# Kernel optimization log

Hardware: AMD Instinct MI355X
Metric: run time of the kernel (lower is better)

## Reference

```python
import jax, jax.numpy as jnp
import numpy as np

N = 100000   # nodes
E = 1600000  # edges per snapshot
S = 4        # snapshots
D = 128      # node_dim
H = 256      # hidden dim
P = 10000    # post nodes


def setup_inputs() -> dict:
    key = jax.random.key(0)
    ks = jax.random.split(key, 11)
    return {
        "node_features": jax.random.normal(ks[0], (N, D), jnp.float32),
        "edge_index": jax.random.randint(ks[1], (S, 2, E), 0, N, dtype=jnp.int32),
        "post_idx": jax.random.randint(ks[2], (P,), 0, N, dtype=jnp.int32),
        "W1": jax.random.normal(ks[3], (D, H), jnp.float32) * (1.0 / np.sqrt(D)),
        "b1": jnp.zeros((H,), jnp.float32),
        "W2": jax.random.normal(ks[4], (H, H), jnp.float32) * (1.0 / np.sqrt(H)),
        "b2": jnp.zeros((H,), jnp.float32),
        "Wc1": jax.random.normal(ks[5], (H, H // 2), jnp.float32) * (1.0 / np.sqrt(H)),
        "bc1": jnp.zeros((H // 2,), jnp.float32),
        "Wc2": jax.random.normal(ks[6], (H // 2, 1), jnp.float32) * (1.0 / np.sqrt(H // 2)),
        "bc2": jnp.zeros((1,), jnp.float32),
    }


def _gcn_conv(x, W, b, src, dst):
    # PyG GCNConv: linear transform, then symmetric-normalized aggregation
    # with self-loops: out_i = sum_j (xW)_j / sqrt(d_i d_j) + (xW)_i / d_i + b
    xw = x @ W                                   # [N, H]
    deg = jnp.ones((N,), xw.dtype).at[dst].add(1.0)  # in-degree + self-loop
    dinv = jax.lax.rsqrt(deg)                    # [N]
    norm = dinv[src] * dinv[dst]                 # [E]
    msg = xw[src] * norm[:, None]                # [E, H] gather + scale
    agg = jax.ops.segment_sum(msg, dst, num_segments=N)  # scatter-add
    agg = agg + xw * (dinv * dinv)[:, None]      # self-loop term
    return agg + b


def reference(node_features, edge_index, post_idx, W1, b1, W2, b2, Wc1, bc1, Wc2, bc2):
    embs = []
    for s in range(S):  # small fixed snapshot loop
        src, dst = edge_index[s, 0], edge_index[s, 1]
        # layer 0: 128->256, relu (dropout identity in eval), no residual (dim change)
        h = jax.nn.relu(_gcn_conv(node_features, W1, b1, src, dst))
        # layer 1 (last): no relu, residual since dims match
        h = _gcn_conv(h, W2, b2, src, dst) + h
        embs.append(h)
    agg = jnp.mean(jnp.stack(embs), axis=0)      # 'mean' snapshot aggregation
    post = agg[post_idx]                         # [P, H]
    hid = jax.nn.relu(post @ Wc1 + bc1)
    logits = (hid @ Wc2 + bc2)[:, 0]
    return jax.nn.sigmoid(logits)
```

## Files before the change

### kernel.cpp

```cpp
#include <hip/hip_runtime.h>
#include <math.h>

#define N_NODES 100000
#define E_EDGES 1600000
#define S_SNAP  4
#define D_IN    128
#define H_DIM   256
#define P_POST  10000
#define SCAN_NBLK ((N_NODES + 255) / 256)
#define NBIN 8
#define BIN_W (N_NODES / NBIN)
#define FILL_CHUNK 2048
#define FILL_NCHUNK ((E_EDGES + FILL_CHUNK - 1) / FILL_CHUNK)

typedef __attribute__((ext_vector_type(8))) short bf16x8;
typedef __attribute__((ext_vector_type(4))) float f32x4;

__device__ __forceinline__ float bf2f(unsigned short u) {
    union { unsigned int i; float f; } v; v.i = ((unsigned int)u) << 16; return v.f;
}
__device__ __forceinline__ unsigned short f2bf(float f) {
    union { float f; unsigned int i; } v; v.f = f;
    unsigned int lsb = (v.i >> 16) & 1u;
    v.i += 0x7fffu + lsb;
    return (unsigned short)(v.i >> 16);
}

__global__ void zero32_kernel(unsigned int* __restrict__ p, int n) {
    int i = blockIdx.x * blockDim.x + threadIdx.x;
    if (i < n) p[i] = 0u;
}

__global__ void hist_kernel(const int* __restrict__ dst, int* __restrict__ deg,
        int* __restrict__ slot) {
    int i = blockIdx.x * blockDim.x + threadIdx.x;
    if (i < E_EDGES) slot[i] = atomicAdd(&deg[dst[i]], 1);
}

__global__ void dinv_kernel(const int* __restrict__ deg, float* __restrict__ dinv) {
    int i = blockIdx.x * blockDim.x + threadIdx.x;
    if (i < N_NODES) dinv[i] = rsqrtf((float)(deg[i] + 1));
}

__global__ __launch_bounds__(256) void scan_part_kernel(const int* __restrict__ deg,
        int* __restrict__ bsum) {
    __shared__ int red[4];
    int i = blockIdx.x * 256 + threadIdx.x;
    int s = (i < N_NODES) ? deg[i] : 0;
    #pragma unroll
    for (int off = 32; off > 0; off >>= 1) s += __shfl_down(s, off, 64);
    int wave = threadIdx.x >> 6, lane = threadIdx.x & 63;
    if (lane == 0) red[wave] = s;
    __syncthreads();
    if (threadIdx.x == 0) bsum[blockIdx.x] = red[0] + red[1] + red[2] + red[3];
}

__global__ __launch_bounds__(512) void scan_top_kernel(const int* __restrict__ bsum,
        int* __restrict__ boff) {
    __shared__ int s[512];
    int t = threadIdx.x;
    s[t] = (t < SCAN_NBLK) ? bsum[t] : 0;
    __syncthreads();
    for (int off = 1; off < 512; off <<= 1) {
        int v = (t >= off) ? s[t - off] : 0;
        __syncthreads();
        s[t] += v;
        __syncthreads();
    }
    if (t < SCAN_NBLK) boff[t] = (t == 0) ? 0 : s[t - 1];
}

__global__ __launch_bounds__(256) void scan_fin_kernel(const int* __restrict__ deg,
        const int* __restrict__ boff, int* __restrict__ rowptr) {
    __shared__ int s[256];
    int b = blockIdx.x, t = threadIdx.x;
    int i = b * 256 + t;
    int v = (i < N_NODES) ? deg[i] : 0;
    s[t] = v;
    __syncthreads();
    for (int off = 1; off < 256; off <<= 1) {
        int u = (t >= off) ? s[t - off] : 0;
        __syncthreads();
        s[t] += u;
        __syncthreads();
    }
    if (i < N_NODES) rowptr[i] = boff[b] + s[t] - v;
    if (i == 0) rowptr[N_NODES] = E_EDGES;
}

__global__ __launch_bounds__(256) void fill_kernel(const int* __restrict__ src,
        const int* __restrict__ dst, const int* __restrict__ slot,
        const int* __restrict__ rowptr, int* __restrict__ csrsrc) {
    int chunk = blockIdx.x >> 3;
    int bin = blockIdx.x & (NBIN - 1);
    int lo = bin * BIN_W, hi = lo + BIN_W;
    int base = chunk * FILL_CHUNK + threadIdx.x;
    #pragma unroll
    for (int k = 0; k < FILL_CHUNK / 256; ++k) {
        int i = base + k * 256;
        if (i < E_EDGES) {
            int d = dst[i];
            if (d >= lo && d < hi) csrsrc[rowptr[d] + slot[i]] = src[i];
        }
    }
}

__global__ __launch_bounds__(256) void gemm_xw1_mfma(const float* __restrict__ A,
        const float* __restrict__ B, unsigned short* __restrict__ C, int M) {
    __shared__ unsigned short As[64][136];
    __shared__ unsigned short Bs[64][136];
    int tid = threadIdx.x;
    int m0 = blockIdx.x * 64, n0 = blockIdx.y * 64;
    {
        int row = tid >> 2, c0 = (tid & 3) * 32;
        int gm = m0 + row;
        #pragma unroll
        for (int i = 0; i < 8; ++i) {
            float4 v = make_float4(0.f, 0.f, 0.f, 0.f);
            if (gm < M) v = *(const float4*)(A + (size_t)gm * D_IN + c0 + i * 4);
            As[row][c0 + i * 4 + 0] = f2bf(v.x);
            As[row][c0 + i * 4 + 1] = f2bf(v.y);
            As[row][c0 + i * 4 + 2] = f2bf(v.z);
            As[row][c0 + i * 4 + 3] = f2bf(v.w);
        }
    }
    {
        int k = tid >> 1, nb = (tid & 1) * 32;
        #pragma unroll
        for (int i = 0; i < 8; ++i) {
            float4 v = *(const float4*)(B + (size_t)k * H_DIM + n0 + nb + i * 4);
            Bs[nb + i * 4 + 0][k] = f2bf(v.x);
            Bs[nb + i * 4 + 1][k] = f2bf(v.y);
            Bs[nb + i * 4 + 2][k] = f2bf(v.z);
            Bs[nb + i * 4 + 3][k] = f2bf(v.w);
        }
    }
    __syncthreads();
    int w = tid >> 6, l = tid & 63;
    int q = l >> 4, mrow = l & 15;
    f32x4 acc[4] = {{0.f,0.f,0.f,0.f},{0.f,0.f,0.f,0.f},{0.f,0.f,0.f,0.f},{0.f,0.f,0.f,0.f}};
    #pragma unroll
    for (int kk = 0; kk < 4; ++kk) {
        bf16x8 a = *(const bf16x8*)&As[16 * w + mrow][kk * 32 + q * 8];
        #pragma unroll
        for (int ct = 0; ct < 4; ++ct) {
            bf16x8 b = *(const bf16x8*)&Bs[ct * 16 + mrow][kk * 32 + q * 8];
            acc[ct] = __builtin_amdgcn_mfma_f32_16x16x32_bf16(a, b, acc[ct], 0, 0, 0);
        }
    }
    #pragma unroll
    for (int ct = 0; ct < 4; ++ct) {
        int col = n0 + ct * 16 + mrow;
        #pragma unroll
        for (int i = 0; i < 4; ++i) {
            int m = m0 + 16 * w + q * 4 + i;
            if (m < M) C[(size_t)m * H_DIM + col] = f2bf(acc[ct][i]);
        }
    }
}

__global__ __launch_bounds__(256) void spmm_l0_kernel(const unsigned short* __restrict__ xw1,
        const float* __restrict__ dinv, const int* __restrict__ rowptr,
        const int* __restrict__ csrsrc, const float* __restrict__ b1,
        unsigned short* __restrict__ h) {
    int r = (blockIdx.x << 2) + (threadIdx.x >> 6);
    int lane = threadIdx.x & 63;
    int e0 = rowptr[r], e1 = rowptr[r + 1];
    float di = dinv[r];
    float4 acc = make_float4(0.f, 0.f, 0.f, 0.f);
    const ushort4* tp = (const ushort4*)xw1;
    int e = e0;
    for (; e + 8 <= e1; e += 8) {
        int s[8]; float wv[8]; ushort4 u[8];
        #pragma unroll
        for (int j = 0; j < 8; ++j) s[j] = csrsrc[e + j];
        #pragma unroll
        for (int j = 0; j < 8; ++j) u[j] = tp[(size_t)s[j] * 64 + lane];
        #pragma unroll
        for (int j = 0; j < 8; ++j) wv[j] = dinv[s[j]] * di;
        #pragma unroll
        for (int j = 0; j < 8; ++j) {
            acc.x = fmaf(bf2f(u[j].x), wv[j], acc.x);
            acc.y = fmaf(bf2f(u[j].y), wv[j], acc.y);
            acc.z = fmaf(bf2f(u[j].z), wv[j], acc.z);
            acc.w = fmaf(bf2f(u[j].w), wv[j], acc.w);
        }
    }
    for (; e < e1; ++e) {
        int s = csrsrc[e];
        float wv = dinv[s] * di;
        ushort4 u = tp[(size_t)s * 64 + lane];
        acc.x = fmaf(bf2f(u.x), wv, acc.x); acc.y = fmaf(bf2f(u.y), wv, acc.y);
        acc.z = fmaf(bf2f(u.z), wv, acc.z); acc.w = fmaf(bf2f(u.w), wv, acc.w);
    }
    ushort4 us = tp[(size_t)r * 64 + lane];
    float wd = di * di;
    float4 bb = ((const float4*)b1)[lane];
    ushort4 o;
    o.x = f2bf(fmaxf(fmaf(bf2f(us.x), wd, acc.x) + bb.x, 0.f));
    o.y = f2bf(fmaxf(fmaf(bf2f(us.y), wd, acc.y) + bb.y, 0.f));
    o.z = f2bf(fmaxf(fmaf(bf2f(us.z), wd, acc.z) + bb.z, 0.f));
    o.w = f2bf(fmaxf(fmaf(bf2f(us.w), wd, acc.w) + bb.w, 0.f));
    ((ushort4*)h)[(size_t)r * 64 + lane] = o;
}

__global__ __launch_bounds__(256) void spmm_h_post_kernel(const unsigned short* __restrict__ h,
        const float* __restrict__ dinv, const int* __restrict__ rowptr,
        const int* __restrict__ csrsrc, const int* __restrict__ post,
        float* __restrict__ t1p) {
    int p = (blockIdx.x << 2) + (threadIdx.x >> 6);
    int lane = threadIdx.x & 63;
    int r = post[p];
    int e0 = rowptr[r], e1 = rowptr[r + 1];
    float di = dinv[r];
    float4 acc = make_float4(0.f, 0.f, 0.f, 0.f);
    const ushort4* hp = (const ushort4*)h;
    int e = e0;
    for (; e + 4 <= e1; e += 4) {
        int s0 = csrsrc[e], s1 = csrsrc[e + 1], s2 = csrsrc[e + 2], s3 = csrsrc[e + 3];
        float w0 = dinv[s0] * di, w1 = dinv[s1] * di, w2 = dinv[s2] * di, w3 = dinv[s3] * di;
        ushort4 u0 = hp[(size_t)s0 * 64 + lane];
        ushort4 u1 = hp[(size_t)s1 * 64 + lane];
        ushort4 u2 = hp[(size_t)s2 * 64 + lane];
        ushort4 u3 = hp[(size_t)s3 * 64 + lane];
        acc.x = fmaf(bf2f(u0.x), w0, acc.x); acc.y = fmaf(bf2f(u0.y), w0, acc.y);
        acc.z = fmaf(bf2f(u0.z), w0, acc.z); acc.w = fmaf(bf2f(u0.w), w0, acc.w);
        acc.x = fmaf(bf2f(u1.x), w1, acc.x); acc.y = fmaf(bf2f(u1.y), w1, acc.y);
        acc.z = fmaf(bf2f(u1.z), w1, acc.z); acc.w = fmaf(bf2f(u1.w), w1, acc.w);
        acc.x = fmaf(bf2f(u2.x), w2, acc.x); acc.y = fmaf(bf2f(u2.y), w2, acc.y);
        acc.z = fmaf(bf2f(u2.z), w2, acc.z); acc.w = fmaf(bf2f(u2.w), w2, acc.w);
        acc.x = fmaf(bf2f(u3.x), w3, acc.x); acc.y = fmaf(bf2f(u3.y), w3, acc.y);
        acc.z = fmaf(bf2f(u3.z), w3, acc.z); acc.w = fmaf(bf2f(u3.w), w3, acc.w);
    }
    for (; e < e1; ++e) {
        int s = csrsrc[e];
        float wv = dinv[s] * di;
        ushort4 u = hp[(size_t)s * 64 + lane];
        acc.x = fmaf(bf2f(u.x), wv, acc.x); acc.y = fmaf(bf2f(u.y), wv, acc.y);
        acc.z = fmaf(bf2f(u.z), wv, acc.z); acc.w = fmaf(bf2f(u.w), wv, acc.w);
    }
    ushort4 u = hp[(size_t)r * 64 + lane];
    float wd = di * di;
    acc.x = fmaf(bf2f(u.x), wd, acc.x);
    acc.y = fmaf(bf2f(u.y), wd, acc.y);
    acc.z = fmaf(bf2f(u.z), wd, acc.z);
    acc.w = fmaf(bf2f(u.w), wd, acc.w);
    ((float4*)t1p)[(size_t)p * 64 + lane] = acc;
}

__global__ __launch_bounds__(256) void gemm_l1_kernel(const float* __restrict__ A,
        const float* __restrict__ B, const float* __restrict__ b2,
        const unsigned short* __restrict__ h, const int* __restrict__ post,
        float* __restrict__ accP, int M) {
    __shared__ float As[16][68];
    __shared__ float Bs[16][68];
    int tid = threadIdx.x;
    int tx = tid & 15, ty = tid >> 4;
    int m0 = blockIdx.x * 64, n0 = blockIdx.y * 64;
    int lar = tid >> 2;
    int lac = (tid & 3) << 2;
    int lbr = tid >> 4;
    int lbc = (tid & 15) << 2;
    float acc[4][4] = {};
    for (int kk = 0; kk < 256; kk += 16) {
        float4 av = make_float4(0.f, 0.f, 0.f, 0.f);
        if (m0 + lar < M) av = *(const float4*)(A + (size_t)(m0 + lar) * 256 + kk + lac);
        float4 bv = *(const float4*)(B + (size_t)(kk + lbr) * 256 + n0 + lbc);
        __syncthreads();
        As[lac + 0][lar] = av.x; As[lac + 1][lar] = av.y;
        As[lac + 2][lar] = av.z; As[lac + 3][lar] = av.w;
        *(float4*)(&Bs[lbr][lbc]) = bv;
        __syncthreads();
        #pragma unroll
        for (int k = 0; k < 16; ++k) {
            float4 a4 = *(const float4*)(&As[k][ty << 2]);
            float4 b4 = *(const float4*)(&Bs[k][tx << 2]);
            float a[4] = {a4.x, a4.y, a4.z, a4.w};
            float b[4] = {b4.x, b4.y, b4.z, b4.w};
            #pragma unroll
            for (int i = 0; i < 4; ++i)
                #pragma unroll
                for (int j = 0; j < 4; ++j)
                    acc[i][j] = fmaf(a[i], b[j], acc[i][j]);
        }
    }
    int nb = n0 + (tx << 2);
    float4 bv = *(const float4*)(b2 + nb);
    float bf[4] = {bv.x, bv.y, bv.z, bv.w};
    #pragma unroll
    for (int i = 0; i < 4; ++i) {
        int m = m0 + (ty << 2) + i;
        if (m < M) {
            int node = post[m];
            ushort4 hr = *(const ushort4*)(h + (size_t)node * 256 + nb);
            float4 a = *(float4*)(accP + (size_t)m * 256 + nb);
            a.x += acc[i][0] + bf[0] + bf2f(hr.x);
            a.y += acc[i][1] + bf[1] + bf2f(hr.y);
            a.z += acc[i][2] + bf[2] + bf2f(hr.z);
            a.w += acc[i][3] + bf[3] + bf2f(hr.w);
            *(float4*)(accP + (size_t)m * 256 + nb) = a;
        }
    }
}

__global__ __launch_bounds__(128) void classifier_kernel(const float* __restrict__ accP,
        const float* __restrict__ Wc1, const float* __restrict__ bc1,
        const float* __restrict__ Wc2, const float* __restrict__ bc2,
        float* __restrict__ out) {
    __shared__ float arow[8][256];
    __shared__ float red[2][8];
    int p0 = blockIdx.x << 3;
    int tid = threadIdx.x;
    for (int idx = tid; idx < 8 * 256; idx += 128) {
        int pl = idx >> 8, k = idx & 255;
        arow[pl][k] = 0.25f * accP[(size_t)(p0 + pl) * 256 + k];
    }
    __syncthreads();
    float s[8];
    float b = bc1[tid];
    #pragma unroll
    for (int pl = 0; pl < 8; ++pl) s[pl] = b;
    for (int k = 0; k < 256; ++k) {
        float wv = Wc1[k * 128 + tid];
        #pragma unroll
        for (int pl = 0; pl < 8; ++pl) s[pl] = fmaf(arow[pl][k], wv, s[pl]);
    }
    float wc2 = Wc2[tid];
    float part[8];
    #pragma unroll
    for (int pl = 0; pl < 8; ++pl) part[pl] = fmaxf(s[pl], 0.f) * wc2;
    #pragma unroll
    for (int off = 32; off > 0; off >>= 1)
        #pragma unroll
        for (int pl = 0; pl < 8; ++pl) part[pl] += __shfl_down(part[pl], off, 64);
    int wave = tid >> 6, lane = tid & 63;
    if (lane == 0) {
        #pragma unroll
        for (int pl = 0; pl < 8; ++pl) red[wave][pl] = part[pl];
    }
    __syncthreads();
    if (tid < 8) {
        float logit = red[0][tid] + red[1][tid] + bc2[0];
        out[p0 + tid] = 1.f / (1.f + expf(-logit));
    }
}

extern "C" void kernel_launch(void* const* d_in, const int* in_sizes, int n_in,
                              void* d_out, int out_size, void* d_ws, size_t ws_size,
                              hipStream_t stream) {
    const float* x   = (const float*)d_in[0];
    const int*   ei  = (const int*)d_in[1];
    const int*   post= (const int*)d_in[2];
    const float* W1  = (const float*)d_in[3];
    const float* b1  = (const float*)d_in[4];
    const float* W2  = (const float*)d_in[5];
    const float* b2  = (const float*)d_in[6];
    const float* Wc1 = (const float*)d_in[7];
    const float* bc1 = (const float*)d_in[8];
    const float* Wc2 = (const float*)d_in[9];
    const float* bc2 = (const float*)d_in[10];
    float* out = (float*)d_out;

    char* w = (char*)d_ws;
    size_t off = 0;
#define WS_ALLOC(type, name, count) \
    type* name = (type*)(w + off); \
    off += (((size_t)(count) * sizeof(type)) + 255) & ~(size_t)255;
    WS_ALLOC(unsigned short, xw1,  (size_t)N_NODES * H_DIM)
    WS_ALLOC(unsigned short, hbuf, (size_t)N_NODES * H_DIM)
    WS_ALLOC(float,          t1p,  (size_t)P_POST * H_DIM)
    WS_ALLOC(float,          accP, (size_t)P_POST * H_DIM)
    WS_ALLOC(int,            deg,    N_NODES)
    WS_ALLOC(float,          dinvb,  N_NODES)
    WS_ALLOC(int,            rowptr, N_NODES + 1)
    WS_ALLOC(int,            csrsrc, E_EDGES)
    WS_ALLOC(int,            bsum,   SCAN_NBLK)
    WS_ALLOC(int,            boff,   SCAN_NBLK)
#undef WS_ALLOC
    int* slot = (int*)t1p;
    (void)ws_size; (void)in_sizes; (void)n_in; (void)out_size;

    zero32_kernel<<<(P_POST * H_DIM + 255) / 256, 256, 0, stream>>>((unsigned int*)accP, P_POST * H_DIM);

    dim3 gg((N_NODES + 63) / 64, H_DIM / 64);
    gemm_xw1_mfma<<<gg, 256, 0, stream>>>(x, W1, xw1, N_NODES);

    for (int s = 0; s < S_SNAP; ++s) {
        const int* srcs = ei + (size_t)s * 2 * E_EDGES;
        const int* dsts = srcs + E_EDGES;
        zero32_kernel<<<(N_NODES + 255) / 256, 256, 0, stream>>>((unsigned int*)deg, N_NODES);
        hist_kernel<<<E_EDGES / 256, 256, 0, stream>>>(dsts, deg, slot);
        dinv_kernel<<<(N_NODES + 255) / 256, 256, 0, stream>>>(deg, dinvb);
        scan_part_kernel<<<SCAN_NBLK, 256, 0, stream>>>(deg, bsum);
        scan_top_kernel<<<1, 512, 0, stream>>>(bsum, boff);
        scan_fin_kernel<<<SCAN_NBLK, 256, 0, stream>>>(deg, boff, rowptr);
        fill_kernel<<<FILL_NCHUNK * NBIN, 256, 0, stream>>>(srcs, dsts, slot, rowptr, csrsrc);
        spmm_l0_kernel<<<N_NODES / 4, 256, 0, stream>>>(xw1, dinvb, rowptr, csrsrc, b1, hbuf);
        spmm_h_post_kernel<<<P_POST / 4, 256, 0, stream>>>(hbuf, dinvb, rowptr, csrsrc, post, t1p);
        dim3 g1((P_POST + 63) / 64, 4);
        gemm_l1_kernel<<<g1, 256, 0, stream>>>(t1p, W2, b2, hbuf, post, accP, P_POST);
    }
    classifier_kernel<<<P_POST / 8, 128, 0, stream>>>(accP, Wc1, bc1, Wc2, bc2, out);
}
```

Before: 1.393 ms.

## Use bf16 MFMA for layer-1 GEMM, fold dinv into scan, reduce spmm unroll

The layer-1 post-node GEMM moves from a scalar fp32 tiled loop to bf16 MFMA 16x16x32 instructions, converting A and W2 to bf16 while staging them into LDS. The dinv computation is folded into the scan partial kernel, which removes one launch per snapshot. The layer-0 SpMM inner loop is unrolled 4 instead of 8, with loads interleaved, to lower register pressure. The GEMM loses precision by rounding its inputs to bf16, and the B transpose stores to LDS may hit bank conflicts.

Measured after the change: 1.332 ms. 1.05x faster.

```diff
diff --git a/kernel.cpp b/kernel.cpp
--- a/kernel.cpp
+++ b/kernel.cpp
@@ -37,20 +37,20 @@
     if (i < E_EDGES) slot[i] = atomicAdd(&deg[dst[i]], 1);
 }
 
-__global__ void dinv_kernel(const int* __restrict__ deg, float* __restrict__ dinv) {
-    int i = blockIdx.x * blockDim.x + threadIdx.x;
-    if (i < N_NODES) dinv[i] = rsqrtf((float)(deg[i] + 1));
-}
-
 __global__ __launch_bounds__(256) void scan_part_kernel(const int* __restrict__ deg,
-        int* __restrict__ bsum) {
+        int* __restrict__ bsum, float* __restrict__ dinv) {
     __shared__ int red[4];
     int i = blockIdx.x * 256 + threadIdx.x;
-    int s = (i < N_NODES) ? deg[i] : 0;
-    #pragma unroll
-    for (int off = 32; off > 0; off >>= 1) s += __shfl_down(s, off, 64);
+    int s = 0;
+    if (i < N_NODES) {
+        s = deg[i];
+        dinv[i] = rsqrtf((float)(s + 1));
+    }
+    int t = s;
+    #pragma unroll
+    for (int off = 32; off > 0; off >>= 1) t += __shfl_down(t, off, 64);
     int wave = threadIdx.x >> 6, lane = threadIdx.x & 63;
-    if (lane == 0) red[wave] = s;
+    if (lane == 0) red[wave] = t;
     __syncthreads();
     if (threadIdx.x == 0) bsum[blockIdx.x] = red[0] + red[1] + red[2] + red[3];
 }
@@ -170,21 +170,21 @@
     float4 acc = make_float4(0.f, 0.f, 0.f, 0.f);
     const ushort4* tp = (const ushort4*)xw1;
     int e = e0;
-    for (; e + 8 <= e1; e += 8) {
-        int s[8]; float wv[8]; ushort4 u[8];
-        #pragma unroll
-        for (int j = 0; j < 8; ++j) s[j] = csrsrc[e + j];
-        #pragma unroll
-        for (int j = 0; j < 8; ++j) u[j] = tp[(size_t)s[j] * 64 + lane];
-        #pragma unroll
-        for (int j = 0; j < 8; ++j) wv[j] = dinv[s[j]] * di;
-        #pragma unroll
-        for (int j = 0; j < 8; ++j) {
-            acc.x = fmaf(bf2f(u[j].x), wv[j], acc.x);
-            acc.y = fmaf(bf2f(u[j].y), wv[j], acc.y);
-            acc.z = fmaf(bf2f(u[j].z), wv[j], acc.z);
-            acc.w = fmaf(bf2f(u[j].w), wv[j], acc.w);
-        }
+    for (; e + 4 <= e1; e += 4) {
+        int s0 = csrsrc[e], s1 = csrsrc[e + 1], s2 = csrsrc[e + 2], s3 = csrsrc[e + 3];
+        float w0 = dinv[s0] * di, w1 = dinv[s1] * di, w2 = dinv[s2] * di, w3 = dinv[s3] * di;
+        ushort4 u0 = tp[(size_t)s0 * 64 + lane];
+        ushort4 u1 = tp[(size_t)s1 * 64 + lane];
+        ushort4 u2 = tp[(size_t)s2 * 64 + lane];
+        ushort4 u3 = tp[(size_t)s3 * 64 + lane];
+        acc.x = fmaf(bf2f(u0.x), w0, acc.x); acc.y = fmaf(bf2f(u0.y), w0, acc.y);
+        acc.z = fmaf(bf2f(u0.z), w0, acc.z); acc.w = fmaf(bf2f(u0.w), w0, acc.w);
+        acc.x = fmaf(bf2f(u1.x), w1, acc.x); acc.y = fmaf(bf2f(u1.y), w1, acc.y);
+        acc.z = fmaf(bf2f(u1.z), w1, acc.z); acc.w = fmaf(bf2f(u1.w), w1, acc.w);
+        acc.x = fmaf(bf2f(u2.x), w2, acc.x); acc.y = fmaf(bf2f(u2.y), w2, acc.y);
+        acc.z = fmaf(bf2f(u2.z), w2, acc.z); acc.w = fmaf(bf2f(u2.w), w2, acc.w);
+        acc.x = fmaf(bf2f(u3.x), w3, acc.x); acc.y = fmaf(bf2f(u3.y), w3, acc.y);
+        acc.z = fmaf(bf2f(u3.z), w3, acc.z); acc.w = fmaf(bf2f(u3.w), w3, acc.w);
     }
     for (; e < e1; ++e) {
         int s = csrsrc[e];
@@ -248,57 +248,66 @@
     ((float4*)t1p)[(size_t)p * 64 + lane] = acc;
 }
 
-__global__ __launch_bounds__(256) void gemm_l1_kernel(const float* __restrict__ A,
+__global__ __launch_bounds__(256) void gemm_l1_mfma(const float* __restrict__ A,
         const float* __restrict__ B, const float* __restrict__ b2,
         const unsigned short* __restrict__ h, const int* __restrict__ post,
         float* __restrict__ accP, int M) {
-    __shared__ float As[16][68];
-    __shared__ float Bs[16][68];
+    __shared__ unsigned short As[64][136];
+    __shared__ unsigned short Bs[64][136];
     int tid = threadIdx.x;
-    int tx = tid & 15, ty = tid >> 4;
     int m0 = blockIdx.x * 64, n0 = blockIdx.y * 64;
-    int lar = tid >> 2;
-    int lac = (tid & 3) << 2;
-    int lbr = tid >> 4;
-    int lbc = (tid & 15) << 2;
-    float acc[4][4] = {};
-    for (int kk = 0; kk < 256; kk += 16) {
-        float4 av = make_float4(0.f, 0.f, 0.f, 0.f);
-        if (m0 + lar < M) av = *(const float4*)(A + (size_t)(m0 + lar) * 256 + kk + lac);
-        float4 bv = *(const float4*)(B + (size_t)(kk + lbr) * 256 + n0 + lbc);
-        __syncthreads();
-        As[lac + 0][lar] = av.x; As[lac + 1][lar] = av.y;
-        As[lac + 2][lar] = av.z; As[lac + 3][lar] = av.w;
-        *(float4*)(&Bs[lbr][lbc]) = bv;
-        __syncthreads();
-        #pragma unroll
-        for (int k = 0; k < 16; ++k) {
-            float4 a4 = *(const float4*)(&As[k][ty << 2]);
-            float4 b4 = *(const float4*)(&Bs[k][tx << 2]);
-            float a[4] = {a4.x, a4.y, a4.z, a4.w};
-            float b[4] = {b4.x, b4.y, b4.z, b4.w};
+    int w = tid >> 6, l = tid & 63;
+    int q = l >> 4, mrow = l & 15;
+    f32x4 acc[4] = {{0.f,0.f,0.f,0.f},{0.f,0.f,0.f,0.f},{0.f,0.f,0.f,0.f},{0.f,0.f,0.f,0.f}};
+    for (int kk = 0; kk < 256; kk += 128) {
+        __syncthreads();
+        {
+            int row = tid >> 2, c0 = (tid & 3) * 32;
+            int gm = m0 + row;
             #pragma unroll
-            for (int i = 0; i < 4; ++i)
-                #pragma unroll
-                for (int j = 0; j < 4; ++j)
-                    acc[i][j] = fmaf(a[i], b[j], acc[i][j]);
-        }
-    }
-    int nb = n0 + (tx << 2);
-    float4 bv = *(const float4*)(b2 + nb);
-    float bf[4] = {bv.x, bv.y, bv.z, bv.w};
-    #pragma unroll
-    for (int i = 0; i < 4; ++i) {
-        int m = m0 + (ty << 2) + i;
-        if (m < M) {
-            int node = post[m];
-            ushort4 hr = *(const ushort4*)(h + (size_t)node * 256 + nb);
-            float4 a = *(float4*)(accP + (size_t)m * 256 + nb);
-            a.x += acc[i][0] + bf[0] + bf2f(hr.x);
-            a.y += acc[i][1] + bf[1] + bf2f(hr.y);
-            a.z += acc[i][2] + bf[2] + bf2f(hr.z);
-            a.w += acc[i][3] + bf[3] + bf2f(hr.w);
-            *(float4*)(accP + (size_t)m * 256 + nb) = a;
+            for (int i = 0; i < 8; ++i) {
+                float4 v = make_float4(0.f, 0.f, 0.f, 0.f);
+                if (gm < M) v = *(const float4*)(A + (size_t)gm * 256 + kk + c0 + i * 4);
+                As[row][c0 + i * 4 + 0] = f2bf(v.x);
+                As[row][c0 + i * 4 + 1] = f2bf(v.y);
+                As[row][c0 + i * 4 + 2] = f2bf(v.z);
+                As[row][c0 + i * 4 + 3] = f2bf(v.w);
+            }
+        }
+        {
+            int k = tid >> 1, nb = (tid & 1) * 32;
+            #pragma unroll
+            for (int i = 0; i < 8; ++i) {
+                float4 v = *(const float4*)(B + (size_t)(kk + k) * H_DIM + n0 + nb + i * 4);
+                Bs[nb + i * 4 + 0][k] = f2bf(v.x);
+                Bs[nb + i * 4 + 1][k] = f2bf(v.y);
+                Bs[nb + i * 4 + 2][k] = f2bf(v.z);
+                Bs[nb + i * 4 + 3][k] = f2bf(v.w);
+            }
+        }
+        __syncthreads();
+        #pragma unroll
+        for (int ks = 0; ks < 4; ++ks) {
+            bf16x8 a = *(const bf16x8*)&As[16 * w + mrow][ks * 32 + q * 8];
+            #pragma unroll
+            for (int ct = 0; ct < 4; ++ct) {
+                bf16x8 b = *(const bf16x8*)&Bs[ct * 16 + mrow][ks * 32 + q * 8];
+                acc[ct] = __builtin_amdgcn_mfma_f32_16x16x32_bf16(a, b, acc[ct], 0, 0, 0);
+            }
+        }
+    }
+    #pragma unroll
+    for (int ct = 0; ct < 4; ++ct) {
+        int col = n0 + ct * 16 + mrow;
+        float bias = b2[col];
+        #pragma unroll
+        for (int i = 0; i < 4; ++i) {
+            int m = m0 + 16 * w + q * 4 + i;
+            if (m < M) {
+                int node = post[m];
+                float hv = bf2f(h[(size_t)node * 256 + col]);
+                accP[(size_t)m * 256 + col] += acc[ct][i] + bias + hv;
+            }
         }
     }
 }
@@ -390,15 +399,14 @@
         const int* dsts = srcs + E_EDGES;
         zero32_kernel<<<(N_NODES + 255) / 256, 256, 0, stream>>>((unsigned int*)deg, N_NODES);
         hist_kernel<<<E_EDGES / 256, 256, 0, stream>>>(dsts, deg, slot);
-        dinv_kernel<<<(N_NODES + 255) / 256, 256, 0, stream>>>(deg, dinvb);
-        scan_part_kernel<<<SCAN_NBLK, 256, 0, stream>>>(deg, bsum);
+        scan_part_kernel<<<SCAN_NBLK, 256, 0, stream>>>(deg, bsum, dinvb);
         scan_top_kernel<<<1, 512, 0, stream>>>(bsum, boff);
         scan_fin_kernel<<<SCAN_NBLK, 256, 0, stream>>>(deg, boff, rowptr);
         fill_kernel<<<FILL_NCHUNK * NBIN, 256, 0, stream>>>(srcs, dsts, slot, rowptr, csrsrc);
         spmm_l0_kernel<<<N_NODES / 4, 256, 0, stream>>>(xw1, dinvb, rowptr, csrsrc, b1, hbuf);
         spmm_h_post_kernel<<<P_POST / 4, 256, 0, stream>>>(hbuf, dinvb, rowptr, csrsrc, post, t1p);
-        dim3 g1((P_POST + 63) / 64, 4);
-        gemm_l1_kernel<<<g1, 256, 0, stream>>>(t1p, W2, b2, hbuf, post, accP, P_POST);
+        dim3 g1((P_POST + 63) / 64, H_DIM / 64);
+        gemm_l1_mfma<<<g1, 256, 0, stream>>>(t1p, W2, b2, hbuf, post, accP, P_POST);
     }
     classifier_kernel<<<P_POST / 8, 128, 0, stream>>>(accP, Wc1, bc1, Wc2, bc2, out);
 }
```
